# Kernel tuning notes

Measured on AMD Instinct MI355X. Metric: run time of the kernel, lower is better.

Reference implementation:

```python
import jax, jax.numpy as jnp
import numpy as np
from jax import lax

# Static configuration (matches init_kwargs / input_specs)
B, DIM, H, W = 4, 192, 64, 64
HEADS, SR, WS = 8, 4, 3
HD = DIM // HEADS            # 24
LL = WS * WS                 # 9  (local window length)
N = H * W                    # 4096 tokens
PH, PW = H // SR, W // SR    # 16, 16 pooled grid
PLEN = PH * PW               # 256
PRETRAIN = 512 // 8          # img_size // 2**(i+2) with i=1 -> 64


def _ln(x, g, b, eps=1e-5):
    m = x.mean(-1, keepdims=True)
    v = ((x - m) ** 2).mean(-1, keepdims=True)
    return (x - m) / jnp.sqrt(v + eps) * g + b


def _l2norm(x):
    n = jnp.sqrt(jnp.sum(x * x, -1, keepdims=True))
    return x / jnp.maximum(n, 1e-12)


def _build_static():
    # get_relative_position_cpb: adaptive 1d pool of arange gives key coords
    qh = np.arange(H, dtype=np.float64)
    qw = np.arange(W, dtype=np.float64)
    kh = qh.reshape(PH, SR).mean(-1)  # H divisible by SR -> uniform bins
    kw = qw.reshape(PW, SR).mean(-1)
    KH, KW = np.meshgrid(kh, kw, indexing='ij')
    QH, QW = np.meshgrid(qh, qw, indexing='ij')
    rel_h = (QH.reshape(-1)[:, None] - KH.reshape(-1)[None, :]) / (PRETRAIN - 1) * 8
    rel_w = (QW.reshape(-1)[:, None] - KW.reshape(-1)[None, :]) / (PRETRAIN - 1) * 8
    rel_hw = np.stack([rel_h, rel_w], -1).reshape(-1, 2)
    table, idx = np.unique(rel_hw, axis=0, return_inverse=True)
    table = np.sign(table) * np.log2(np.abs(table) + 1.0) / np.log2(8.0)
    # get_seqlen_and_mask: validity of each of the 9 neighbors per position
    hh, ww = np.meshgrid(np.arange(H), np.arange(W), indexing='ij')
    hh, ww = hh.reshape(-1), ww.reshape(-1)
    valid = np.stack([(hh + dh >= 0) & (hh + dh < H) & (ww + dw >= 0) & (ww + dw < W)
                      for dh in (-1, 0, 1) for dw in (-1, 0, 1)], -1)  # [N, 9]
    pad_mask = ~valid
    seq_scale = np.log(valid.sum(-1, keepdims=True).astype(np.float64) + PLEN).astype(np.float32)  # [N,1]
    return idx.reshape(-1).astype(np.int32), table.astype(np.float32), seq_scale, pad_mask


def setup_inputs() -> dict:
    key = jax.random.key(0)
    ks = jax.random.split(key, 12)
    f32 = jnp.float32

    def tn(k, shape, std=0.02):
        return jax.random.truncated_normal(k, -2.0, 2.0, shape, f32) * std

    rel_idx, table, seq_scale, pad_mask = _build_static()
    return dict(
        x=jax.random.normal(ks[0], (B, DIM, H, W), f32),
        pe_w=tn(ks[1], (DIM, DIM, 3, 3)),
        pe_b=jnp.zeros((DIM,), f32),
        pe_ln_g=jnp.ones((DIM,), f32), pe_ln_b=jnp.zeros((DIM,), f32),
        q_w=tn(ks[2], (DIM, DIM)), q_b=jnp.zeros((DIM,), f32),
        kv_w=tn(ks[3], (2 * DIM, DIM)), kv_b=jnp.zeros((2 * DIM,), f32),
        sr_w=tn(ks[4], (DIM, DIM)), sr_b=jnp.zeros((DIM,), f32),
        norm_g=jnp.ones((DIM,), f32), norm_b=jnp.zeros((DIM,), f32),
        cpb1_w=tn(ks[5], (512, 2), 0.1), cpb1_b=jnp.zeros((512,), f32),
        cpb2_w=tn(ks[6], (HEADS, 512), 0.05), cpb2_b=jnp.zeros((HEADS,), f32),
        rpb_local=tn(ks[7], (HEADS, LL), 0.0004),
        learnable_tokens=tn(ks[8], (HEADS, HD, LL)),
        learnable_bias=jnp.zeros((HEADS, 1, LL), f32),
        query_embedding=tn(ks[9], (HEADS, 1, HD)),
        temperature=jnp.full((HEADS, 1, 1), float(np.log(np.exp(1.0 / 0.24) - 1.0)), f32),
        proj_w=tn(ks[10], (DIM, DIM)), proj_b=jnp.zeros((DIM,), f32),
        out_ln_g=jnp.ones((DIM,), f32), out_ln_b=jnp.zeros((DIM,), f32),
        rel_idx=jnp.asarray(rel_idx),
        coords_table=jnp.asarray(table),
        seq_scale=jnp.asarray(seq_scale),
        pad_mask=jnp.asarray(pad_mask),
    )


def _forward(x, pe_w, pe_b, pe_ln_g, pe_ln_b, q_w, q_b, kv_w, kv_b, sr_w, sr_b,
             norm_g, norm_b, cpb1_w, cpb1_b, cpb2_w, cpb2_b, rpb_local,
             learnable_tokens, learnable_bias, query_embedding, temperature,
             proj_w, proj_b, out_ln_g, out_ln_b,
             rel_idx, coords_table, seq_scale, pad_mask):
    # OverlapPatchEmbed: 3x3 conv s1 p1 -> tokens -> LN
    xc = lax.conv_general_dilated(x, pe_w, (1, 1), ((1, 1), (1, 1)),
                                  dimension_numbers=('NCHW', 'OIHW', 'NCHW')) + pe_b[None, :, None, None]
    t = _ln(xc.reshape(B, DIM, N).transpose(0, 2, 1), pe_ln_g, pe_ln_b)  # [B,N,C]

    # queries
    q = t @ q_w.T + q_b
    q_norm = _l2norm(q.reshape(B, N, HEADS, HD).transpose(0, 2, 1, 3))   # [B,h,N,d]
    q_scaled = (q_norm + query_embedding[None]) * jax.nn.softplus(temperature)[None] * seq_scale

    # local KV via 3x3 neighborhood gather (torch nn.Unfold)
    kv = t @ kv_w.T + kv_b                                               # [B,N,2C]
    k_loc = _l2norm(kv[..., :DIM].reshape(B, N, HEADS, HD)).reshape(B, N, DIM)
    kv_map = jnp.concatenate([k_loc, kv[..., DIM:]], -1).transpose(0, 2, 1).reshape(B, 2 * DIM, H, W)
    p = jnp.pad(kv_map, ((0, 0), (0, 0), (1, 1), (1, 1)))
    neigh = jnp.stack([p[:, :, kh:kh + H, kw:kw + W] for kh in range(WS) for kw in range(WS)], 2)
    neigh = neigh.reshape(B, 2 * HEADS, HD, LL, N).transpose(0, 1, 4, 2, 3)  # [B,2h,N,d,9]
    k_local, v_local = neigh[:, :HEADS], neigh[:, HEADS:]
    attn_local = jnp.einsum('bhnd,bhndl->bhnl', q_scaled, k_local) + rpb_local[None, :, None, :]
    attn_local = jnp.where(pad_mask[None, None], -jnp.inf, attn_local)   # [B,h,N,9]

    # pooled global KV: 1x1 conv -> GELU -> adaptive avg pool -> LN -> kv
    x_map = t.transpose(0, 2, 1).reshape(B, DIM, H, W)
    sr_out = jax.nn.gelu(jnp.einsum('oc,bchw->bohw', sr_w, x_map) + sr_b[None, :, None, None],
                         approximate=False)
    pooled = sr_out.reshape(B, DIM, PH, SR, PW, SR).mean((3, 5)).reshape(B, DIM, PLEN).transpose(0, 2, 1)
    pooled = _ln(pooled, norm_g, norm_b)
    kv_p = (pooled @ kv_w.T + kv_b).reshape(B, PLEN, 2 * HEADS, HD).transpose(0, 2, 1, 3)
    k_pool, v_pool = kv_p[:, :HEADS], kv_p[:, HEADS:]

    # CPB relative position bias for the pooled branch
    cpb = jax.nn.relu(coords_table @ cpb1_w.T + cpb1_b) @ cpb2_w.T + cpb2_b  # [T,h]
    pool_bias = cpb.T[:, rel_idx].reshape(HEADS, N, PLEN)
    attn_pool = jnp.einsum('bhnd,bhmd->bhnm', q_scaled, _l2norm(k_pool)) + pool_bias[None]

    # joint softmax over local + pooled keys
    attn = jax.nn.softmax(jnp.concatenate([attn_local, attn_pool], -1), -1)
    a_loc, a_pool = attn[..., :LL], attn[..., LL:]

    w_loc = jnp.einsum('bhnd,hdl->bhnl', q_norm, learnable_tokens) + learnable_bias[None] + a_loc
    x_local = jnp.einsum('bhnl,bhndl->bhnd', w_loc, v_local)
    x_pool = jnp.einsum('bhnm,bhmd->bhnd', a_pool, v_pool)

    out = (x_local + x_pool).transpose(0, 2, 1, 3).reshape(B, N, DIM) @ proj_w.T + proj_b
    out = _ln(out, out_ln_g, out_ln_b)
    return out.transpose(0, 2, 1).reshape(B, DIM, H, W)


def reference(x, pe_w, pe_b, pe_ln_g, pe_ln_b, q_w, q_b, kv_w, kv_b, sr_w, sr_b,
              norm_g, norm_b, cpb1_w, cpb1_b, cpb2_w, cpb2_b, rpb_local,
              learnable_tokens, learnable_bias, query_embedding, temperature,
              proj_w, proj_b, out_ln_g, out_ln_b,
              rel_idx, coords_table, seq_scale, pad_mask):
    return _forward(x, pe_w, pe_b, pe_ln_g, pe_ln_b, q_w, q_b, kv_w, kv_b, sr_w, sr_b,
                    norm_g, norm_b, cpb1_w, cpb1_b, cpb2_w, cpb2_b, rpb_local,
                    learnable_tokens, learnable_bias, query_embedding, temperature,
                    proj_w, proj_b, out_ln_g, out_ln_b,
                    rel_idx, coords_table, seq_scale, pad_mask)
```

## Files before the change

kernel.cpp:

```cpp
#include <hip/hip_runtime.h>
#include <stdint.h>


__device__ __forceinline__ float b2f(unsigned short u) {
  return __uint_as_float(((unsigned)u) << 16);
}
__device__ __forceinline__ unsigned short f2b(float f) {
  unsigned x = __float_as_uint(f);
  return (unsigned short)((x + 0x7fffu + ((x >> 16) & 1u)) >> 16);
}

constexpr size_t OFF_T    = 0;
constexpr size_t OFF_KMAP = 3145728;
constexpr size_t OFF_QN   = 9437184;
constexpr size_t OFF_QS   = 12582912;
constexpr size_t OFF_CTX  = 15728640;
constexpr size_t OFF_POOL = 18874368;
constexpr size_t OFF_KP   = 19070976;
constexpr size_t OFF_VP   = 19267584;
constexpr size_t OFF_CPB  = 19464192;
constexpr size_t OFF_BIAS = 19595264;
constexpr size_t OFF_WTC  = OFF_CTX;
constexpr size_t OFF_QT   = OFF_CTX + 331776;
constexpr size_t OFF_KVT  = OFF_CTX + 368640;
constexpr size_t OFF_SRT  = OFF_CTX + 442368;
constexpr size_t OFF_PJT  = OFF_KMAP;

__global__ __launch_bounds__(256) void k_wt_conv(const float* __restrict__ pw,
                                                 float* __restrict__ wt) {
  int i = blockIdx.x * 256 + threadIdx.x;
  if (i >= 331776) return;
  int oc = i % 192, k = i / 192;
  wt[i] = pw[(size_t)oc * 1728 + k];
}
__global__ __launch_bounds__(256) void k_wt_gen(const float* __restrict__ src,
                                                float* __restrict__ dst, int O, int K) {
  int i = blockIdx.x * 256 + threadIdx.x;
  if (i >= O * K) return;
  int o = i % O, k = i / O;
  dst[i] = src[(size_t)o * K + k];
}

__global__ __launch_bounds__(256) void k_conv(
    const float* __restrict__ x, const float* __restrict__ wtc,
    float* __restrict__ p0, float* __restrict__ p1, float* __restrict__ p2,
    float* __restrict__ p3, float* __restrict__ p4, float* __restrict__ p5) {
  __shared__ float xl[8 * 6 * 66];
  const int tid = threadIdx.x;
  const int lane = tid & 63;
  const int wv = __builtin_amdgcn_readfirstlane(tid >> 6);
  const int h0 = blockIdx.x * 4;
  const int b = blockIdx.y;
  const int zz = blockIdx.z;
  const int obase = (zz & 3) * 48;
  const int ith = zz >> 2;
  const int icb = ith * 4;
  const int ow = obase + wv * 12;

  float acc[4][12];
#pragma unroll
  for (int ro = 0; ro < 4; ++ro)
#pragma unroll
    for (int j = 0; j < 12; ++j) acc[ro][j] = 0.f;

  float xr[13];
  auto loadx = [&](int ic0) {
#pragma unroll
    for (int s = 0; s < 13; ++s) {
      int f = tid + s * 256;
      float v = 0.f;
      if (f < 3168) {
        int ii = f / 396;
        int rem = f - ii * 396;
        int r = rem / 66;
        int wp = rem - r * 66;
        int hh = h0 + r - 1, ww = wp - 1;
        if (hh >= 0 && hh < 64 && ww >= 0 && ww < 64)
          v = x[((size_t)(b * 192 + ic0 * 8 + ii) << 12) + (hh << 6) + ww];
      }
      xr[s] = v;
    }
  };
  loadx(icb);

  for (int i2 = 0; i2 < 4; ++i2) {
    const int ic0 = icb + i2;
    __syncthreads();
#pragma unroll
    for (int s = 0; s < 13; ++s) {
      int f = tid + s * 256;
      if (f < 3168) {
        int ii = f / 396;
        int rem = f - ii * 396;
        int r = rem / 66;
        int wp = rem - r * 66;
        xl[(ii * 6 + r) * 66 + wp] = xr[s];
      }
    }
    __syncthreads();
    if (i2 < 3) loadx(ic0 + 1);
    const float* wb = wtc + (size_t)ic0 * 72 * 192 + ow;
#pragma unroll 1
    for (int ii = 0; ii < 8; ++ii) {
      float xv[6][3];
#pragma unroll
      for (int r6 = 0; r6 < 6; ++r6) {
        const float* xp = &xl[(ii * 6 + r6) * 66 + lane];
        xv[r6][0] = xp[0]; xv[r6][1] = xp[1]; xv[r6][2] = xp[2];
      }
#pragma unroll
      for (int kh = 0; kh < 3; ++kh) {
#pragma unroll
        for (int kw = 0; kw < 3; ++kw) {
          const float4* wp = (const float4*)(wb + (size_t)(ii * 9 + kh * 3 + kw) * 192);
          float4 wA = wp[0], wB = wp[1], wC = wp[2];
#pragma unroll
          for (int ro = 0; ro < 4; ++ro) {
            float xvv = xv[ro + kh][kw];
            acc[ro][0]  += xvv * wA.x;
            acc[ro][1]  += xvv * wA.y;
            acc[ro][2]  += xvv * wA.z;
            acc[ro][3]  += xvv * wA.w;
            acc[ro][4]  += xvv * wB.x;
            acc[ro][5]  += xvv * wB.y;
            acc[ro][6]  += xvv * wB.z;
            acc[ro][7]  += xvv * wB.w;
            acc[ro][8]  += xvv * wC.x;
            acc[ro][9]  += xvv * wC.y;
            acc[ro][10] += xvv * wC.z;
            acc[ro][11] += xvv * wC.w;
          }
        }
      }
    }
  }
  float* tdst = (ith == 0) ? p0 : (ith == 1) ? p1 : (ith == 2) ? p2
              : (ith == 3) ? p3 : (ith == 4) ? p4 : p5;
#pragma unroll
  for (int ro = 0; ro < 4; ++ro) {
    float* op = tdst + ((size_t)b * 4096 + (h0 + ro) * 64 + lane) * 192 + ow;
#pragma unroll
    for (int j4 = 0; j4 < 3; ++j4) {
      float4 v;
      v.x = acc[ro][j4 * 4 + 0];
      v.y = acc[ro][j4 * 4 + 1];
      v.z = acc[ro][j4 * 4 + 2];
      v.w = acc[ro][j4 * 4 + 3];
      ((float4*)op)[j4] = v;
    }
  }
}

__global__ __launch_bounds__(256) void k_ln_rows(float* __restrict__ data,
    const float* __restrict__ d2, const float* __restrict__ d3,
    const float* __restrict__ d4, const float* __restrict__ d5,
    const float* __restrict__ d6, const float* __restrict__ cbias,
    const float* __restrict__ g, const float* __restrict__ be, int rows) {
  int lane = threadIdx.x & 63;
  int wv = threadIdx.x >> 6;
  int row = blockIdx.x * 4 + wv;
  if (row >= rows) return;
  float* p = data + (size_t)row * 192;
  float v0 = p[lane], v1 = p[lane + 64], v2 = p[lane + 128];
  if (d2) {
    const float* q = d2 + (size_t)row * 192;
    v0 += q[lane]; v1 += q[lane + 64]; v2 += q[lane + 128];
  }
  if (d3) {
    const float* q = d3 + (size_t)row * 192;
    v0 += q[lane]; v1 += q[lane + 64]; v2 += q[lane + 128];
  }
  if (d4) {
    const float* q = d4 + (size_t)row * 192;
    v0 += q[lane]; v1 += q[lane + 64]; v2 += q[lane + 128];
  }
  if (d5) {
    const float* q = d5 + (size_t)row * 192;
    v0 += q[lane]; v1 += q[lane + 64]; v2 += q[lane + 128];
  }
  if (d6) {
    const float* q = d6 + (size_t)row * 192;
    v0 += q[lane]; v1 += q[lane + 64]; v2 += q[lane + 128];
  }
  if (cbias) {
    v0 += cbias[lane]; v1 += cbias[lane + 64]; v2 += cbias[lane + 128];
  }
  float s = v0 + v1 + v2;
  float sq = v0 * v0 + v1 * v1 + v2 * v2;
#pragma unroll
  for (int m = 32; m >= 1; m >>= 1) {
    s += __shfl_xor(s, m, 64);
    sq += __shfl_xor(sq, m, 64);
  }
  float mean = s * (1.f / 192.f);
  float var = sq * (1.f / 192.f) - mean * mean;
  float rstd = rsqrtf(var + 1e-5f);
  p[lane]       = (v0 - mean) * rstd * g[lane]       + be[lane];
  p[lane + 64]  = (v1 - mean) * rstd * g[lane + 64]  + be[lane + 64];
  p[lane + 128] = (v2 - mean) * rstd * g[lane + 128] + be[lane + 128];
}

template <int OCB, typename GXV, typename GXD>
__device__ __forceinline__ void gemm_tiles(
    float* __restrict__ wl, float* __restrict__ xs, int tid, int lane, int wv,
    const float* __restrict__ wt, int ostr, int obase,
    float (&acc)[OCB / 4], GXV gxv, GXD gxd) {
  constexpr int NPF4 = OCB / 4;
  constexpr int NW4 = OCB / 16;
  constexpr int NWR = (32 * NPF4 + 255) / 256;
  constexpr bool WEXACT = (32 * NPF4 % 256) == 0;
  float xr[8];
  float4 wr[NWR];
  auto loadx = [&](int k0) {
#pragma unroll
    for (int s = 0; s < 8; ++s) xr[s] = gxv(k0, tid + s * 256);
  };
  auto loadw = [&](int k0) {
#pragma unroll
    for (int s = 0; s < NWR; ++s) {
      int f4 = tid + s * 256;
      if (WEXACT || f4 < 32 * NPF4) {
        int kk = f4 / NPF4, j = f4 - kk * NPF4;
        wr[s] = ((const float4*)(wt + (size_t)(k0 + kk) * ostr + obase))[j];
      }
    }
  };
  loadx(0); loadw(0);
  for (int kt = 0; kt < 6; ++kt) {
    __syncthreads();
#pragma unroll
    for (int s = 0; s < 8; ++s) xs[gxd(tid + s * 256)] = xr[s];
#pragma unroll
    for (int s = 0; s < NWR; ++s) {
      int f4 = tid + s * 256;
      if (WEXACT || f4 < 32 * NPF4) ((float4*)wl)[f4] = wr[s];
    }
    __syncthreads();
    if (kt < 5) { loadx((kt + 1) * 32); loadw((kt + 1) * 32); }
#pragma unroll 4
    for (int kk = 0; kk < 32; ++kk) {
      float xv = xs[kk * 66 + lane];
      const float4* wrow = (const float4*)&wl[kk * OCB + wv * NW4 * 4];
#pragma unroll
      for (int j4 = 0; j4 < NW4; ++j4) {
        float4 w4 = wrow[j4];
        acc[j4 * 4 + 0] += xv * w4.x;
        acc[j4 * 4 + 1] += xv * w4.y;
        acc[j4 * 4 + 2] += xv * w4.z;
        acc[j4 * 4 + 3] += xv * w4.w;
      }
    }
  }
}

__global__ __launch_bounds__(256) void k_q(
    const float* __restrict__ t, const float* __restrict__ qt, const float* __restrict__ qb,
    const float* __restrict__ qe, const float* __restrict__ tmp, const float* __restrict__ ss,
    float* __restrict__ qno, float* __restrict__ qso) {
  __shared__ __align__(16) float wl[32 * 96];
  __shared__ float xs[32 * 66];
  const int tid = threadIdx.x;
  const int lane = tid & 63;
  const int wv = __builtin_amdgcn_readfirstlane(tid >> 6);
  const int n0 = blockIdx.x * 64;
  const int b = blockIdx.y;
  const int obase = blockIdx.z * 96;
  const int hh = blockIdx.z * 4 + wv;
  const int oc0 = obase + wv * 24;
  float acc[24];
#pragma unroll
  for (int j = 0; j < 24; ++j) acc[j] = 0.f;

  gemm_tiles<96>(wl, xs, tid, lane, wv, qt, 192, obase, acc,
    [&](int k0, int f) {
      int nl = f >> 5, kk = f & 31;
      return t[((size_t)b * 4096 + n0 + nl) * 192 + k0 + kk];
    },
    [&](int f) { return (f & 31) * 66 + (f >> 5); });

  const int n = n0 + lane;
  float ssv = ss[n];
  float sumsq = 0.f;
#pragma unroll
  for (int d = 0; d < 24; ++d) {
    float v = acc[d] + qb[oc0 + d];
    sumsq += v * v;
  }
  float rn = 1.f / fmaxf(sqrtf(sumsq), 1e-12f);
  float sp = log1pf(__expf(tmp[hh]));
#pragma unroll
  for (int d = 0; d < 24; ++d) {
    float qv = (acc[d] + qb[oc0 + d]) * rn;
    size_t o = ((size_t)(b * 8 + hh) * 24 + d) * 4096 + n;
    qno[o] = qv;
    qso[o] = (qv + qe[hh * 24 + d]) * sp * ssv;
  }
}

__global__ __launch_bounds__(256) void k_kv(
    const float* __restrict__ t, const float* __restrict__ kvt, const float* __restrict__ kb_,
    float* __restrict__ kmap) {
  __shared__ __align__(16) float wl[32 * 96];
  __shared__ float xs[32 * 66];
  const int tid = threadIdx.x;
  const int lane = tid & 63;
  const int wv = __builtin_amdgcn_readfirstlane(tid >> 6);
  const int n0 = blockIdx.x * 64;
  const int b = blockIdx.y;
  const int obase = blockIdx.z * 96;
  const int oc0 = obase + wv * 24;
  const int n = n0 + lane;
  float acc[24];
#pragma unroll
  for (int j = 0; j < 24; ++j) acc[j] = 0.f;

  gemm_tiles<96>(wl, xs, tid, lane, wv, kvt, 384, obase, acc,
    [&](int k0, int f) {
      int nl = f >> 5, kk = f & 31;
      return t[((size_t)b * 4096 + n0 + nl) * 192 + k0 + kk];
    },
    [&](int f) { return (f & 31) * 66 + (f >> 5); });

  if (oc0 < 192) {
    float sumsq = 0.f;
#pragma unroll
    for (int d = 0; d < 24; ++d) {
      float v = acc[d] + kb_[oc0 + d];
      sumsq += v * v;
    }
    float rn = 1.f / fmaxf(sqrtf(sumsq), 1e-12f);
#pragma unroll
    for (int d = 0; d < 24; ++d)
      kmap[((size_t)b * 384 + oc0 + d) * 4096 + n] = (acc[d] + kb_[oc0 + d]) * rn;
  } else {
#pragma unroll
    for (int d = 0; d < 24; ++d)
      kmap[((size_t)b * 384 + oc0 + d) * 4096 + n] = acc[d] + kb_[oc0 + d];
  }
}

__device__ __forceinline__ float gelu_exact(float v) {
  float u = v * 0.70710678118654752f;
  float a = fabsf(u);
  float tt = 1.f / (1.f + 0.3275911f * a);
  float poly = ((((1.061405429f * tt - 1.453152027f) * tt + 1.421413741f) * tt
                 - 0.284496736f) * tt + 0.254829592f) * tt;
  float erfa = 1.f - poly * __expf(-a * a);
  float erfv = (u < 0.f) ? -erfa : erfa;
  return 0.5f * v * (1.f + erfv);
}

__global__ __launch_bounds__(256) void k_srpool(
    const float* __restrict__ t, const float* __restrict__ srt, const float* __restrict__ sb,
    float* __restrict__ pooled) {
  __shared__ __align__(16) float wl[32 * 48];
  __shared__ float xs[32 * 66];
  const int tid = threadIdx.x;
  const int lane = tid & 63;
  const int wv = __builtin_amdgcn_readfirstlane(tid >> 6);
  const int wx = blockIdx.x & 3;
  const int obase = (blockIdx.x >> 2) * 48;
  const int ph = blockIdx.y;
  const int b = blockIdx.z;
  const int oc0 = obase + wv * 12;
  float acc[12];
#pragma unroll
  for (int j = 0; j < 12; ++j) acc[j] = 0.f;

  gemm_tiles<48>(wl, xs, tid, lane, wv, srt, 192, obase, acc,
    [&](int k0, int f) {
      int pl = f >> 5, kk = f & 31;
      int row = (ph * 4 + (pl >> 4)) * 64 + wx * 16 + (pl & 15);
      return t[((size_t)b * 4096 + row) * 192 + k0 + kk];
    },
    [&](int f) { return (f & 31) * 66 + (f >> 5); });

#pragma unroll
  for (int j = 0; j < 12; ++j) {
    float gv = gelu_exact(acc[j] + sb[oc0 + j]);
    gv += __shfl_xor(gv, 1, 64);
    gv += __shfl_xor(gv, 2, 64);
    gv += __shfl_xor(gv, 16, 64);
    gv += __shfl_xor(gv, 32, 64);
    if ((lane & 51) == 0) {
      int cell = (lane >> 2) & 3;
      int p = ph * 16 + wx * 4 + cell;
      pooled[((size_t)b * 256 + p) * 192 + oc0 + j] = gv * (1.f / 16.f);
    }
  }
}

__global__ __launch_bounds__(256) void k_kvp(
    const float* __restrict__ pooled, const float* __restrict__ kvt, const float* __restrict__ kb_,
    float* __restrict__ kp, float* __restrict__ vp) {
  __shared__ __align__(16) float wl[32 * 96];
  __shared__ float xs[32 * 66];
  const int tid = threadIdx.x;
  const int lane = tid & 63;
  const int wv = __builtin_amdgcn_readfirstlane(tid >> 6);
  const int r0 = blockIdx.x * 64;
  const int obase = blockIdx.y * 96;
  const int oc0 = obase + wv * 24;
  const int row = r0 + lane;
  const int b = row >> 8;
  const int m = row & 255;
  float acc[24];
#pragma unroll
  for (int j = 0; j < 24; ++j) acc[j] = 0.f;

  gemm_tiles<96>(wl, xs, tid, lane, wv, kvt, 384, obase, acc,
    [&](int k0, int f) {
      int nl = f >> 5, kk = f & 31;
      return pooled[(size_t)(r0 + nl) * 192 + k0 + kk];
    },
    [&](int f) { return (f & 31) * 66 + (f >> 5); });

  if (oc0 < 192) {
    int hh = oc0 / 24;
    float sumsq = 0.f;
#pragma unroll
    for (int d = 0; d < 24; ++d) {
      float v = acc[d] + kb_[oc0 + d];
      sumsq += v * v;
    }
    float rn = 1.f / fmaxf(sqrtf(sumsq), 1e-12f);
#pragma unroll
    for (int d = 0; d < 24; ++d)
      kp[(((size_t)(b * 8 + hh)) * 256 + m) * 24 + d] = (acc[d] + kb_[oc0 + d]) * rn;
  } else {
    int hh = (oc0 - 192) / 24;
#pragma unroll
    for (int d = 0; d < 24; ++d)
      vp[(((size_t)(b * 8 + hh)) * 256 + m) * 24 + d] = acc[d] + kb_[oc0 + d];
  }
}

__global__ __launch_bounds__(256) void k_cpb(
    const float* __restrict__ coords, const float* __restrict__ c1w,
    const float* __restrict__ c1b, const float* __restrict__ c2w,
    const float* __restrict__ c2b, float* __restrict__ cpb, int T) {
  __shared__ float s1w[1024];
  __shared__ float s1b[512];
  __shared__ __align__(16) float s2w[512 * 8];
  const int tid = threadIdx.x;
  for (int f = tid; f < 1024; f += 256) s1w[f] = c1w[f];
  for (int f = tid; f < 512; f += 256) s1b[f] = c1b[f];
  for (int f = tid; f < 4096; f += 256) {
    int h = f >> 9, j = f & 511;
    s2w[j * 8 + h] = c2w[f];
  }
  __syncthreads();
  int i = blockIdx.x * 256 + tid;
  int ic = (i < T) ? i : (T - 1);
  float x0 = coords[2 * ic], y0 = coords[2 * ic + 1];
  float a[8];
#pragma unroll
  for (int h = 0; h < 8; ++h) a[h] = c2b[h];
#pragma unroll 4
  for (int j = 0; j < 512; ++j) {
    float hv = fmaxf(s1w[2 * j] * x0 + s1w[2 * j + 1] * y0 + s1b[j], 0.f);
    const float4* w2 = (const float4*)&s2w[j * 8];
    float4 wA = w2[0], wB = w2[1];
    a[0] += hv * wA.x; a[1] += hv * wA.y; a[2] += hv * wA.z; a[3] += hv * wA.w;
    a[4] += hv * wB.x; a[5] += hv * wB.y; a[6] += hv * wB.z; a[7] += hv * wB.w;
  }
  if (i < T) {
#pragma unroll
    for (int h = 0; h < 8; ++h) cpb[(size_t)i * 8 + h] = a[h];
  }
}

__global__ __launch_bounds__(256) void k_bias(
    const int* __restrict__ rel, const float* __restrict__ cpb,
    unsigned short* __restrict__ bt) {
  int g = blockIdx.x * 256 + threadIdx.x;
  int n = g >> 5;
  int m0 = (g & 31) * 8;
  const int4* r4 = (const int4*)(rel + (size_t)n * 256 + m0);
  int4 ra = r4[0], rb = r4[1];
  int idxs[8] = {ra.x, ra.y, ra.z, ra.w, rb.x, rb.y, rb.z, rb.w};
  unsigned acc[8][4];
#pragma unroll
  for (int j = 0; j < 8; ++j) {
    const float4* c4 = (const float4*)(cpb + (size_t)idxs[j] * 8);
    float4 A = c4[0], Bv = c4[1];
    float vals[8] = {A.x, A.y, A.z, A.w, Bv.x, Bv.y, Bv.z, Bv.w};
#pragma unroll
    for (int hh = 0; hh < 8; ++hh) {
      unsigned u = f2b(vals[hh]);
      if (j & 1) acc[hh][j >> 1] |= u << 16;
      else       acc[hh][j >> 1]  = u;
    }
  }
#pragma unroll
  for (int hh = 0; hh < 8; ++hh) {
    uint4 o;
    o.x = acc[hh][0]; o.y = acc[hh][1]; o.z = acc[hh][2]; o.w = acc[hh][3];
    *(uint4*)(bt + ((size_t)hh * 4096 + n) * 256 + m0) = o;
  }
}

__global__ __launch_bounds__(512, 4) void k_attn(
    const float* __restrict__ qs_g, const float* __restrict__ qn_g,
    const float* __restrict__ kmap, const float* __restrict__ kp, const float* __restrict__ vp,
    const unsigned short* __restrict__ bt, const float* __restrict__ rpb,
    const float* __restrict__ lt, const float* __restrict__ lb,
    float* __restrict__ ctx) {
  __shared__ __align__(16) float smem[12288];
  float* kl = smem;
  float* vl = smem + 6144;
  const int tid = threadIdx.x;
  const int lane = tid & 63;
  const int w = __builtin_amdgcn_readfirstlane(tid >> 6);
  const int qm = w & 3;
  const int rr = w >> 2;
  const int row = blockIdx.x * 2 + rr;
  const int h = blockIdx.y;
  const int b = blockIdx.z;
  const int n = (row << 6) + lane;
  const float SHIFT = 15.f;

  {
    const float4* kps = (const float4*)(kp + (size_t)(b * 8 + h) * 6144);
    const float4* vps = (const float4*)(vp + (size_t)(b * 8 + h) * 6144);
    float4* kld = (float4*)kl;
    float4* vld = (float4*)vl;
#pragma unroll
    for (int c = 0; c < 3; ++c) {
      int f = tid + c * 512;
      kld[f] = kps[f];
      vld[f] = vps[f];
    }
  }

  float qsv[24];
  {
    const float* qsb = qs_g + ((size_t)(b * 8 + h) * 24) * 4096 + n;
#pragma unroll
    for (int d = 0; d < 24; ++d) qsv[d] = qsb[(size_t)d * 4096];
  }

  const int l0 = (qm == 1) ? 0 : ((qm == 0) ? 3 : (qm * 2 + 1));
  const int lcnt = (qm == 1) ? 3 : 2;

  float wlv[3];
  {
    float qnv[24];
    const float* qnb = qn_g + ((size_t)(b * 8 + h) * 24) * 4096 + n;
#pragma unroll
    for (int d = 0; d < 24; ++d) qnv[d] = qnb[(size_t)d * 4096];
    const float* ltp = lt + h * 216;
    const float* lbp = lb + h * 9;
#pragma unroll
    for (int j = 0; j < 3; ++j) {
      float a = 0.f;
      if (j < lcnt) {
        int l = l0 + j;
#pragma unroll
        for (int d = 0; d < 24; ++d) a += qnv[d] * ltp[d * 9 + l];
        a += lbp[l];
      }
      wlv[j] = a;
    }
  }

  float ctxA[24], ctxBP[24];
#pragma unroll
  for (int d = 0; d < 24; ++d) { ctxA[d] = 0.f; ctxBP[d] = 0.f; }
  float S = 0.f;

  {
    const float* kbase = kmap + ((size_t)b * 384 + h * 24) * 4096;
    const float* rpp = rpb + h * 9;
    for (int j = 0; j < lcnt; ++j) {
      const int l = l0 + j;
      const int dh = l / 3 - 1, dw = l % 3 - 1;
      const int hp = row + dh;
      if (hp < 0 || hp >= 64) continue;
      const int wp2 = lane + dw;
      const bool okw = (wp2 >= 0) && (wp2 < 64);
      const int nn = (hp << 6) + (okw ? wp2 : lane);
      const float* kb = kbase + nn;
      const float* vb = kb + (size_t)192 * 4096;
      float d0 = 0, d1 = 0, d2 = 0, d3 = 0;
#pragma unroll
      for (int d = 0; d < 24; d += 4) {
        d0 += qsv[d] * kb[(size_t)d * 4096];
        d1 += qsv[d + 1] * kb[(size_t)(d + 1) * 4096];
        d2 += qsv[d + 2] * kb[(size_t)(d + 2) * 4096];
        d3 += qsv[d + 3] * kb[(size_t)(d + 3) * 4096];
      }
      float p = okw ? __expf((d0 + d1) + (d2 + d3) + rpp[l] - SHIFT) : 0.f;
      S += p;
      float wll = okw ? wlv[j] : 0.f;
#pragma unroll
      for (int d = 0; d < 24; ++d) {
        float vv = vb[(size_t)d * 4096];
        ctxA[d] += wll * vv;
        ctxBP[d] += p * vv;
      }
    }
  }

  __syncthreads();

  {
    const unsigned short* bp = bt + ((size_t)h * 4096 + n) * 256 + qm * 64;
    const float* klq = kl + qm * (64 * 24);
    const float* vlq = vl + qm * (64 * 24);
    uint4 bcur = *(const uint4*)bp;
#pragma unroll 1
    for (int c = 0; c < 8; ++c) {
      uint4 bnx = bcur;
      if (c < 7) bnx = *(const uint4*)(bp + (c + 1) * 8);
#pragma unroll
      for (int j = 0; j < 8; ++j) {
        const float4* kr4 = (const float4*)&klq[(c * 8 + j) * 24];
        const float4* vr4 = (const float4*)&vlq[(c * 8 + j) * 24];
        float d0 = 0, d1 = 0, d2 = 0, d3 = 0;
#pragma unroll
        for (int q4 = 0; q4 < 6; ++q4) {
          float4 k4 = kr4[q4];
          d0 += qsv[q4 * 4 + 0] * k4.x;
          d1 += qsv[q4 * 4 + 1] * k4.y;
          d2 += qsv[q4 * 4 + 2] * k4.z;
          d3 += qsv[q4 * 4 + 3] * k4.w;
        }
        unsigned word = (j < 2) ? bcur.x : (j < 4) ? bcur.y : (j < 6) ? bcur.z : bcur.w;
        float bv = (j & 1) ? __uint_as_float(word & 0xffff0000u)
                           : __uint_as_float(word << 16);
        float p = __expf((d0 + d1) + (d2 + d3) + bv - SHIFT);
        S += p;
#pragma unroll
        for (int q4 = 0; q4 < 6; ++q4) {
          float4 v4 = vr4[q4];
          ctxBP[q4 * 4 + 0] += p * v4.x;
          ctxBP[q4 * 4 + 1] += p * v4.y;
          ctxBP[q4 * 4 + 2] += p * v4.z;
          ctxBP[q4 * 4 + 3] += p * v4.w;
        }
      }
      bcur = bnx;
    }
  }

  for (int src = 1; src < 4; ++src) {
    __syncthreads();
    if (qm == src) {
      float* p = smem + (size_t)(rr * 64 + lane) * 49;
      p[0] = S;
#pragma unroll
      for (int d = 0; d < 24; ++d) { p[1 + d] = ctxA[d]; p[25 + d] = ctxBP[d]; }
    }
    __syncthreads();
    if (qm == 0) {
      const float* p = smem + (size_t)(rr * 64 + lane) * 49;
      S += p[0];
#pragma unroll
      for (int d = 0; d < 24; ++d) { ctxA[d] += p[1 + d]; ctxBP[d] += p[25 + d]; }
    }
  }
  if (qm == 0) {
    const float inv = 1.f / S;
    float* cb = ctx + ((size_t)(b * 8 + h) * 24) * 4096 + n;
#pragma unroll
    for (int d = 0; d < 24; ++d)
      cb[(size_t)d * 4096] = ctxA[d] + ctxBP[d] * inv;
  }
}

__global__ __launch_bounds__(256) void k_projg(
    const float* __restrict__ ctx, const float* __restrict__ pjt, const float* __restrict__ pb,
    float* __restrict__ pout) {
  __shared__ __align__(16) float wl[32 * 96];
  __shared__ float xs[32 * 66];
  const int tid = threadIdx.x;
  const int lane = tid & 63;
  const int wv = __builtin_amdgcn_readfirstlane(tid >> 6);
  const int n0 = blockIdx.x * 64;
  const int b = blockIdx.y;
  const int obase = blockIdx.z * 96;
  const int oc0 = obase + wv * 24;
  const int n = n0 + lane;
  float acc[24];
#pragma unroll
  for (int j = 0; j < 24; ++j) acc[j] = 0.f;

  gemm_tiles<96>(wl, xs, tid, lane, wv, pjt, 192, obase, acc,
    [&](int k0, int f) {
      int kk = f >> 6, nl = f & 63;
      return ctx[((size_t)b * 192 + k0 + kk) * 4096 + n0 + nl];
    },
    [&](int f) { return (f >> 6) * 66 + (f & 63); });

#pragma unroll
  for (int d = 0; d < 24; ++d)
    pout[((size_t)b * 192 + oc0 + d) * 4096 + n] = acc[d] + pb[oc0 + d];
}

__global__ __launch_bounds__(256) void k_oln(
    const float* __restrict__ pout, const float* __restrict__ g,
    const float* __restrict__ be, float* __restrict__ out) {
  __shared__ float red[2][4][64];
  const int tid = threadIdx.x;
  const int lane = tid & 63;
  const int wv = __builtin_amdgcn_readfirstlane(tid >> 6);
  const int n0 = blockIdx.x * 64;
  const int b = blockIdx.y;
  const int o0 = wv * 48;
  float v[48];
  float s = 0.f, sq = 0.f;
#pragma unroll
  for (int j = 0; j < 48; ++j) {
    v[j] = pout[((size_t)b * 192 + o0 + j) * 4096 + n0 + lane];
    s += v[j];
    sq += v[j] * v[j];
  }
  red[0][wv][lane] = s;
  red[1][wv][lane] = sq;
  __syncthreads();
  float st = red[0][0][lane] + red[0][1][lane] + red[0][2][lane] + red[0][3][lane];
  float sqt = red[1][0][lane] + red[1][1][lane] + red[1][2][lane] + red[1][3][lane];
  float mean = st * (1.f / 192.f);
  float var = sqt * (1.f / 192.f) - mean * mean;
  float rstd = rsqrtf(var + 1e-5f);
#pragma unroll
  for (int j = 0; j < 48; ++j) {
    int o = o0 + j;
    out[((size_t)b * 192 + o) * 4096 + n0 + lane] = (v[j] - mean) * rstd * g[o] + be[o];
  }
}

extern "C" void kernel_launch(void* const* d_in, const int* in_sizes, int n_in,
                              void* d_out, int out_size, void* d_ws, size_t ws_size,
                              hipStream_t stream) {
  float* w = (float*)d_ws;

  const float* x      = (const float*)d_in[0];
  const float* pe_w   = (const float*)d_in[1];
  const float* pe_b   = (const float*)d_in[2];
  const float* peln_g = (const float*)d_in[3];
  const float* peln_b = (const float*)d_in[4];
  const float* q_w    = (const float*)d_in[5];
  const float* q_b    = (const float*)d_in[6];
  const float* kv_w   = (const float*)d_in[7];
  const float* kv_b   = (const float*)d_in[8];
  const float* sr_w   = (const float*)d_in[9];
  const float* sr_b   = (const float*)d_in[10];
  const float* norm_g = (const float*)d_in[11];
  const float* norm_b = (const float*)d_in[12];
  const float* cpb1w  = (const float*)d_in[13];
  const float* cpb1b  = (const float*)d_in[14];
  const float* cpb2w  = (const float*)d_in[15];
  const float* cpb2b  = (const float*)d_in[16];
  const float* rpb    = (const float*)d_in[17];
  const float* lt     = (const float*)d_in[18];
  const float* lb     = (const float*)d_in[19];
  const float* qe     = (const float*)d_in[20];
  const float* temp   = (const float*)d_in[21];
  const float* proj_w = (const float*)d_in[22];
  const float* proj_b = (const float*)d_in[23];
  const float* oln_g  = (const float*)d_in[24];
  const float* oln_b  = (const float*)d_in[25];
  const int*   rel    = (const int*)d_in[26];
  const float* coords = (const float*)d_in[27];
  const float* ss     = (const float*)d_in[28];

  dim3 blk(256);
  k_wt_conv<<<dim3(1296), blk, 0, stream>>>(pe_w, w + OFF_WTC);
  k_wt_gen<<<dim3(144), blk, 0, stream>>>(q_w, w + OFF_QT, 192, 192);
  k_wt_gen<<<dim3(288), blk, 0, stream>>>(kv_w, w + OFF_KVT, 384, 192);
  k_wt_gen<<<dim3(144), blk, 0, stream>>>(sr_w, w + OFF_SRT, 192, 192);

  k_conv<<<dim3(16, 4, 24), blk, 0, stream>>>(x, w + OFF_WTC,
      w + OFF_T, w + OFF_KMAP, w + OFF_KMAP + 3145728,
      w + OFF_QN, w + OFF_QS, (float*)(w + OFF_BIAS));
  k_ln_rows<<<dim3(4096), blk, 0, stream>>>(w + OFF_T, w + OFF_KMAP,
      w + OFF_KMAP + 3145728, w + OFF_QN, w + OFF_QS, (const float*)(w + OFF_BIAS),
      pe_b, peln_g, peln_b, 16384);
  k_q<<<dim3(64, 4, 2), blk, 0, stream>>>(w + OFF_T, w + OFF_QT, q_b, qe, temp, ss,
      w + OFF_QN, w + OFF_QS);
  k_kv<<<dim3(64, 4, 4), blk, 0, stream>>>(w + OFF_T, w + OFF_KVT, kv_b, w + OFF_KMAP);
  k_srpool<<<dim3(16, 16, 4), blk, 0, stream>>>(w + OFF_T, w + OFF_SRT, sr_b, w + OFF_POOL);
  k_ln_rows<<<dim3(256), blk, 0, stream>>>(w + OFF_POOL, nullptr, nullptr, nullptr,
      nullptr, nullptr, nullptr, norm_g, norm_b, 1024);
  k_kvp<<<dim3(16, 4), blk, 0, stream>>>(w + OFF_POOL, w + OFF_KVT, kv_b,
      w + OFF_KP, w + OFF_VP);
  int T = in_sizes[27] / 2;
  k_cpb<<<dim3((T + 255) / 256), blk, 0, stream>>>(coords, cpb1w, cpb1b, cpb2w, cpb2b,
      w + OFF_CPB, T);
  k_bias<<<dim3(512), blk, 0, stream>>>(rel, w + OFF_CPB,
      (unsigned short*)(w + OFF_BIAS));
  k_attn<<<dim3(32, 8, 4), dim3(512), 0, stream>>>(w + OFF_QS, w + OFF_QN, w + OFF_KMAP,
      w + OFF_KP, w + OFF_VP, (const unsigned short*)(w + OFF_BIAS), rpb, lt, lb,
      w + OFF_CTX);
  k_wt_gen<<<dim3(144), blk, 0, stream>>>(proj_w, w + OFF_PJT, 192, 192);
  k_projg<<<dim3(64, 4, 2), blk, 0, stream>>>(w + OFF_CTX, w + OFF_PJT, proj_b,
      w + OFF_QN);
  k_oln<<<dim3(64, 4), blk, 0, stream>>>(w + OFF_QN, oln_g, oln_b, (float*)d_out);
}
```

Before: 606.5 us.

## Halve conv split-K partials and read GEMM weights directly from global

The conv now splits the input channels into 3 partial sums of 8 chunks each instead of 6 of 4. This halves the grid z-dimension and the partial buffers that the LayerNorm kernel must read and sum. Separately, the shared GEMM tile helper no longer stages weight tiles in LDS and instead reads float4 weights straight from global memory (cached) in the inner loop. That cuts shared memory use and the per-tile copies, but the inner loop now depends on L1/L2 latency, and the conv has fewer blocks for parallelism.

```diff
diff --git a/kernel.cpp b/kernel.cpp
--- a/kernel.cpp
+++ b/kernel.cpp
@@ -43,8 +43,7 @@
 
 __global__ __launch_bounds__(256) void k_conv(
     const float* __restrict__ x, const float* __restrict__ wtc,
-    float* __restrict__ p0, float* __restrict__ p1, float* __restrict__ p2,
-    float* __restrict__ p3, float* __restrict__ p4, float* __restrict__ p5) {
+    float* __restrict__ p0, float* __restrict__ p1, float* __restrict__ p2) {
   __shared__ float xl[8 * 6 * 66];
   const int tid = threadIdx.x;
   const int lane = tid & 63;
@@ -54,7 +53,7 @@
   const int zz = blockIdx.z;
   const int obase = (zz & 3) * 48;
   const int ith = zz >> 2;
-  const int icb = ith * 4;
+  const int icb = ith * 8;
   const int ow = obase + wv * 12;
 
   float acc[4][12];
@@ -83,7 +82,7 @@
   };
   loadx(icb);
 
-  for (int i2 = 0; i2 < 4; ++i2) {
+  for (int i2 = 0; i2 < 8; ++i2) {
     const int ic0 = icb + i2;
     __syncthreads();
 #pragma unroll
@@ -98,7 +97,7 @@
       }
     }
     __syncthreads();
-    if (i2 < 3) loadx(ic0 + 1);
+    if (i2 < 7) loadx(ic0 + 1);
     const float* wb = wtc + (size_t)ic0 * 72 * 192 + ow;
 #pragma unroll 1
     for (int ii = 0; ii < 8; ++ii) {
@@ -134,8 +133,7 @@
       }
     }
   }
-  float* tdst = (ith == 0) ? p0 : (ith == 1) ? p1 : (ith == 2) ? p2
-              : (ith == 3) ? p3 : (ith == 4) ? p4 : p5;
+  float* tdst = (ith == 0) ? p0 : ((ith == 1) ? p1 : p2);
 #pragma unroll
   for (int ro = 0; ro < 4; ++ro) {
     float* op = tdst + ((size_t)b * 4096 + (h0 + ro) * 64 + lane) * 192 + ow;
@@ -152,9 +150,8 @@
 }
 
 __global__ __launch_bounds__(256) void k_ln_rows(float* __restrict__ data,
-    const float* __restrict__ d2, const float* __restrict__ d3,
-    const float* __restrict__ d4, const float* __restrict__ d5,
-    const float* __restrict__ d6, const float* __restrict__ cbias,
+    const float* __restrict__ data2, const float* __restrict__ data3,
+    const float* __restrict__ cbias,
     const float* __restrict__ g, const float* __restrict__ be, int rows) {
   int lane = threadIdx.x & 63;
   int wv = threadIdx.x >> 6;
@@ -162,24 +159,12 @@
   if (row >= rows) return;
   float* p = data + (size_t)row * 192;
   float v0 = p[lane], v1 = p[lane + 64], v2 = p[lane + 128];
-  if (d2) {
-    const float* q = d2 + (size_t)row * 192;
+  if (data2) {
+    const float* q = data2 + (size_t)row * 192;
     v0 += q[lane]; v1 += q[lane + 64]; v2 += q[lane + 128];
   }
-  if (d3) {
-    const float* q = d3 + (size_t)row * 192;
-    v0 += q[lane]; v1 += q[lane + 64]; v2 += q[lane + 128];
-  }
-  if (d4) {
-    const float* q = d4 + (size_t)row * 192;
-    v0 += q[lane]; v1 += q[lane + 64]; v2 += q[lane + 128];
-  }
-  if (d5) {
-    const float* q = d5 + (size_t)row * 192;
-    v0 += q[lane]; v1 += q[lane + 64]; v2 += q[lane + 128];
-  }
-  if (d6) {
-    const float* q = d6 + (size_t)row * 192;
+  if (data3) {
+    const float* q = data3 + (size_t)row * 192;
     v0 += q[lane]; v1 += q[lane + 64]; v2 += q[lane + 128];
   }
   if (cbias) {
@@ -202,45 +187,27 @@
 
 template <int OCB, typename GXV, typename GXD>
 __device__ __forceinline__ void gemm_tiles(
-    float* __restrict__ wl, float* __restrict__ xs, int tid, int lane, int wv,
+    float* __restrict__ xs, int tid, int lane, int wv,
     const float* __restrict__ wt, int ostr, int obase,
     float (&acc)[OCB / 4], GXV gxv, GXD gxd) {
-  constexpr int NPF4 = OCB / 4;
   constexpr int NW4 = OCB / 16;
-  constexpr int NWR = (32 * NPF4 + 255) / 256;
-  constexpr bool WEXACT = (32 * NPF4 % 256) == 0;
   float xr[8];
-  float4 wr[NWR];
   auto loadx = [&](int k0) {
 #pragma unroll
     for (int s = 0; s < 8; ++s) xr[s] = gxv(k0, tid + s * 256);
   };
-  auto loadw = [&](int k0) {
-#pragma unroll
-    for (int s = 0; s < NWR; ++s) {
-      int f4 = tid + s * 256;
-      if (WEXACT || f4 < 32 * NPF4) {
-        int kk = f4 / NPF4, j = f4 - kk * NPF4;
-        wr[s] = ((const float4*)(wt + (size_t)(k0 + kk) * ostr + obase))[j];
-      }
-    }
-  };
-  loadx(0); loadw(0);
+  loadx(0);
   for (int kt = 0; kt < 6; ++kt) {
     __syncthreads();
 #pragma unroll
     for (int s = 0; s < 8; ++s) xs[gxd(tid + s * 256)] = xr[s];
-#pragma unroll
-    for (int s = 0; s < NWR; ++s) {
-      int f4 = tid + s * 256;
-      if (WEXACT || f4 < 32 * NPF4) ((float4*)wl)[f4] = wr[s];
-    }
     __syncthreads();
-    if (kt < 5) { loadx((kt + 1) * 32); loadw((kt + 1) * 32); }
+    if (kt < 5) loadx((kt + 1) * 32);
+    const float* wbase = wt + (size_t)kt * 32 * ostr + obase + wv * (NW4 * 4);
 #pragma unroll 4
     for (int kk = 0; kk < 32; ++kk) {
       float xv = xs[kk * 66 + lane];
-      const float4* wrow = (const float4*)&wl[kk * OCB + wv * NW4 * 4];
+      const float4* wrow = (const float4*)(wbase + (size_t)kk * ostr);
 #pragma unroll
       for (int j4 = 0; j4 < NW4; ++j4) {
         float4 w4 = wrow[j4];
@@ -257,7 +224,6 @@
     const float* __restrict__ t, const float* __restrict__ qt, const float* __restrict__ qb,
     const float* __restrict__ qe, const float* __restrict__ tmp, const float* __restrict__ ss,
     float* __restrict__ qno, float* __restrict__ qso) {
-  __shared__ __align__(16) float wl[32 * 96];
   __shared__ float xs[32 * 66];
   const int tid = threadIdx.x;
   const int lane = tid & 63;
@@ -271,7 +237,7 @@
 #pragma unroll
   for (int j = 0; j < 24; ++j) acc[j] = 0.f;
 
-  gemm_tiles<96>(wl, xs, tid, lane, wv, qt, 192, obase, acc,
+  gemm_tiles<96>(xs, tid, lane, wv, qt, 192, obase, acc,
     [&](int k0, int f) {
       int nl = f >> 5, kk = f & 31;
       return t[((size_t)b * 4096 + n0 + nl) * 192 + k0 + kk];
@@ -300,7 +266,6 @@
 __global__ __launch_bounds__(256) void k_kv(
     const float* __restrict__ t, const float* __restrict__ kvt, const float* __restrict__ kb_,
     float* __restrict__ kmap) {
-  __shared__ __align__(16) float wl[32 * 96];
   __shared__ float xs[32 * 66];
   const int tid = threadIdx.x;
   const int lane = tid & 63;
@@ -314,7 +279,7 @@
 #pragma unroll
   for (int j = 0; j < 24; ++j) acc[j] = 0.f;
 
-  gemm_tiles<96>(wl, xs, tid, lane, wv, kvt, 384, obase, acc,
+  gemm_tiles<96>(xs, tid, lane, wv, kvt, 384, obase, acc,
     [&](int k0, int f) {
       int nl = f >> 5, kk = f & 31;
       return t[((size_t)b * 4096 + n0 + nl) * 192 + k0 + kk];
@@ -353,7 +318,6 @@
 __global__ __launch_bounds__(256) void k_srpool(
     const float* __restrict__ t, const float* __restrict__ srt, const float* __restrict__ sb,
     float* __restrict__ pooled) {
-  __shared__ __align__(16) float wl[32 * 48];
   __shared__ float xs[32 * 66];
   const int tid = threadIdx.x;
   const int lane = tid & 63;
@@ -367,7 +331,7 @@
 #pragma unroll
   for (int j = 0; j < 12; ++j) acc[j] = 0.f;
 
-  gemm_tiles<48>(wl, xs, tid, lane, wv, srt, 192, obase, acc,
+  gemm_tiles<48>(xs, tid, lane, wv, srt, 192, obase, acc,
     [&](int k0, int f) {
       int pl = f >> 5, kk = f & 31;
       int row = (ph * 4 + (pl >> 4)) * 64 + wx * 16 + (pl & 15);
@@ -393,7 +357,6 @@
 __global__ __launch_bounds__(256) void k_kvp(
     const float* __restrict__ pooled, const float* __restrict__ kvt, const float* __restrict__ kb_,
     float* __restrict__ kp, float* __restrict__ vp) {
-  __shared__ __align__(16) float wl[32 * 96];
   __shared__ float xs[32 * 66];
   const int tid = threadIdx.x;
   const int lane = tid & 63;
@@ -408,7 +371,7 @@
 #pragma unroll
   for (int j = 0; j < 24; ++j) acc[j] = 0.f;
 
-  gemm_tiles<96>(wl, xs, tid, lane, wv, kvt, 384, obase, acc,
+  gemm_tiles<96>(xs, tid, lane, wv, kvt, 384, obase, acc,
     [&](int k0, int f) {
       int nl = f >> 5, kk = f & 31;
       return pooled[(size_t)(r0 + nl) * 192 + k0 + kk];
@@ -672,7 +635,6 @@
 __global__ __launch_bounds__(256) void k_projg(
     const float* __restrict__ ctx, const float* __restrict__ pjt, const float* __restrict__ pb,
     float* __restrict__ pout) {
-  __shared__ __align__(16) float wl[32 * 96];
   __shared__ float xs[32 * 66];
   const int tid = threadIdx.x;
   const int lane = tid & 63;
@@ -686,7 +648,7 @@
 #pragma unroll
   for (int j = 0; j < 24; ++j) acc[j] = 0.f;
 
-  gemm_tiles<96>(wl, xs, tid, lane, wv, pjt, 192, obase, acc,
+  gemm_tiles<96>(xs, tid, lane, wv, pjt, 192, obase, acc,
     [&](int k0, int f) {
       int kk = f >> 6, nl = f & 63;
       return ctx[((size_t)b * 192 + k0 + kk) * 4096 + n0 + nl];
@@ -772,18 +734,16 @@
   k_wt_gen<<<dim3(288), blk, 0, stream>>>(kv_w, w + OFF_KVT, 384, 192);
   k_wt_gen<<<dim3(144), blk, 0, stream>>>(sr_w, w + OFF_SRT, 192, 192);
 
-  k_conv<<<dim3(16, 4, 24), blk, 0, stream>>>(x, w + OFF_WTC,
-      w + OFF_T, w + OFF_KMAP, w + OFF_KMAP + 3145728,
-      w + OFF_QN, w + OFF_QS, (float*)(w + OFF_BIAS));
+  k_conv<<<dim3(16, 4, 12), blk, 0, stream>>>(x, w + OFF_WTC, w + OFF_T,
+      w + OFF_KMAP, w + OFF_KMAP + 3145728);
   k_ln_rows<<<dim3(4096), blk, 0, stream>>>(w + OFF_T, w + OFF_KMAP,
-      w + OFF_KMAP + 3145728, w + OFF_QN, w + OFF_QS, (const float*)(w + OFF_BIAS),
-      pe_b, peln_g, peln_b, 16384);
+      w + OFF_KMAP + 3145728, pe_b, peln_g, peln_b, 16384);
   k_q<<<dim3(64, 4, 2), blk, 0, stream>>>(w + OFF_T, w + OFF_QT, q_b, qe, temp, ss,
       w + OFF_QN, w + OFF_QS);
   k_kv<<<dim3(64, 4, 4), blk, 0, stream>>>(w + OFF_T, w + OFF_KVT, kv_b, w + OFF_KMAP);
   k_srpool<<<dim3(16, 16, 4), blk, 0, stream>>>(w + OFF_T, w + OFF_SRT, sr_b, w + OFF_POOL);
   k_ln_rows<<<dim3(256), blk, 0, stream>>>(w + OFF_POOL, nullptr, nullptr, nullptr,
-      nullptr, nullptr, nullptr, norm_g, norm_b, 1024);
+      norm_g, norm_b, 1024);
   k_kvp<<<dim3(16, 4), blk, 0, stream>>>(w + OFF_POOL, w + OFF_KVT, kv_b,
       w + OFF_KP, w + OFF_VP);
   int T = in_sizes[27] / 2;
```

New measurement: 533.6 us. 1.14x faster.
